# Optimization experiments

Measured on AMD Instinct MI355X. Metric: run time of the kernel, lower is better.

Reference implementation:

```python
import jax, jax.numpy as jnp
import numpy as np

N, C = 16384, 1000


def setup_inputs() -> dict:
    key = jax.random.key(0)
    ks = jax.random.split(key, 10)
    inp = {}
    for i in range(8):
        inp[f"outputs{i+1}"] = jax.random.normal(ks[i], (N, C), dtype=jnp.float32)
    inp["mimic"] = jax.random.normal(ks[8], (N, C), dtype=jnp.float32)
    inp["targets"] = jax.random.randint(ks[9], (N,), 0, C, dtype=jnp.int64)
    inp["n_test"] = N
    return inp


def _margin(x, targets):
    # top-2 margin, zeroed when target is not the argmax value
    top2, _ = jax.lax.top_k(x, 2)                      # [N, 2]
    tgt = jnp.take_along_axis(x, targets[:, None], axis=1)[:, 0]  # [N]
    return jnp.where(tgt == top2[:, 0], top2[:, 0] - top2[:, 1],
                     jnp.zeros((), x.dtype))


def reference(outputs1, outputs2, outputs3, outputs4, outputs5, outputs6,
              outputs7, outputs8, mimic, targets, n_test):
    T = 2.0
    outs = [outputs1, outputs2, outputs3, outputs4,
            outputs5, outputs6, outputs7, outputs8, mimic]
    margins = jnp.stack([_margin(o, targets) for o in outs], axis=1)  # [N, 9]
    out_threshold = jax.nn.softmax(margins / T, axis=1)               # [N, 9]
    max_preds = jnp.max(jnp.stack(outs[:8], axis=0))                  # scalar
    return (max_preds, out_threshold)
```

## Files before the change

### kernel.cpp

```cpp
#include <hip/hip_runtime.h>
#include <math.h>

#define BLOCK 256
#define WPB   (BLOCK / 64)

__global__ __launch_bounds__(BLOCK) void margin_kernel(
    const float* __restrict__ o0, const float* __restrict__ o1,
    const float* __restrict__ o2, const float* __restrict__ o3,
    const float* __restrict__ o4, const float* __restrict__ o5,
    const float* __restrict__ o6, const float* __restrict__ o7,
    const float* __restrict__ o8,
    const int* __restrict__ targets,
    float* __restrict__ out, float* __restrict__ block_max,
    int N, int C)
{
    __shared__ float s_m1[WPB][12];
    __shared__ float s_m2[WPB][12];

    const int tid  = threadIdx.x;
    const int lane = tid & 63;
    const int wib  = tid >> 6;
    const int row  = blockIdx.x;
    const int nf4  = C >> 2;
    const unsigned rowoff = (unsigned)row * (unsigned)C;

    float tvv = 0.0f;
    if (wib == 0 && lane < 9) {
        const int c = targets[row];
        const float* tp = o0;
        tp = (lane == 1) ? o1 : tp;  tp = (lane == 2) ? o2 : tp;
        tp = (lane == 3) ? o3 : tp;  tp = (lane == 4) ? o4 : tp;
        tp = (lane == 5) ? o5 : tp;  tp = (lane == 6) ? o6 : tp;
        tp = (lane == 7) ? o7 : tp;  tp = (lane == 8) ? o8 : tp;
        tvv = tp[rowoff + c];
    }

    float m1[9], m2[9];
    #pragma unroll
    for (int k = 0; k < 9; ++k) { m1[k] = -INFINITY; m2[k] = -INFINITY; }

    const float4* p[9] = {
        (const float4*)(o0 + rowoff), (const float4*)(o1 + rowoff),
        (const float4*)(o2 + rowoff), (const float4*)(o3 + rowoff),
        (const float4*)(o4 + rowoff), (const float4*)(o5 + rowoff),
        (const float4*)(o6 + rowoff), (const float4*)(o7 + rowoff),
        (const float4*)(o8 + rowoff) };

    for (int f4 = tid; f4 < nf4; f4 += BLOCK) {
        float4 v[9];
        #pragma unroll
        for (int k = 0; k < 9; ++k) v[k] = p[k][f4];
        #pragma unroll
        for (int k = 0; k < 9; ++k) {
            m2[k] = fmaxf(m2[k], fminf(m1[k], v[k].x)); m1[k] = fmaxf(m1[k], v[k].x);
            m2[k] = fmaxf(m2[k], fminf(m1[k], v[k].y)); m1[k] = fmaxf(m1[k], v[k].y);
            m2[k] = fmaxf(m2[k], fminf(m1[k], v[k].z)); m1[k] = fmaxf(m1[k], v[k].z);
            m2[k] = fmaxf(m2[k], fminf(m1[k], v[k].w)); m1[k] = fmaxf(m1[k], v[k].w);
        }
    }
    if (C & 3) {
        const float* b[9] = {o0,o1,o2,o3,o4,o5,o6,o7,o8};
        for (int idx = (nf4 << 2) + tid; idx < C; idx += BLOCK) {
            #pragma unroll
            for (int k = 0; k < 9; ++k) {
                float v = b[k][rowoff + idx];
                m2[k] = fmaxf(m2[k], fminf(m1[k], v)); m1[k] = fmaxf(m1[k], v);
            }
        }
    }

    #pragma unroll
    for (int off = 32; off > 0; off >>= 1) {
        #pragma unroll
        for (int k = 0; k < 9; ++k) {
            float a1 = __shfl_xor(m1[k], off);
            float a2 = __shfl_xor(m2[k], off);
            m2[k] = fmaxf(fmaxf(m2[k], a2), fminf(m1[k], a1));
            m1[k] = fmaxf(m1[k], a1);
        }
    }

    if (lane == 0) {
        #pragma unroll
        for (int k = 0; k < 9; ++k) { s_m1[wib][k] = m1[k]; s_m2[wib][k] = m2[k]; }
    }
    __syncthreads();

    if (wib == 0) {
        float a1 = -INFINITY, a2 = -INFINITY;
        if (lane < 9) {
            a1 = s_m1[0][lane]; a2 = s_m2[0][lane];
            #pragma unroll
            for (int w = 1; w < WPB; ++w) {
                float b1 = s_m1[w][lane], b2 = s_m2[w][lane];
                a2 = fmaxf(fmaxf(a2, b2), fminf(a1, b1));
                a1 = fmaxf(a1, b1);
            }
        }
        float mg = (lane < 9) ? ((tvv == a1) ? (a1 - a2) : 0.0f) : -INFINITY;

        float mm = mg;
        #pragma unroll
        for (int off = 8; off > 0; off >>= 1) mm = fmaxf(mm, __shfl_xor(mm, off));
        float ex = (lane < 9) ? expf((mg - mm) * 0.5f) : 0.0f;
        float sum = ex;
        #pragma unroll
        for (int off = 8; off > 0; off >>= 1) sum += __shfl_xor(sum, off);
        if (lane < 9)
            out[1 + (size_t)row * 9 + lane] = ex / sum;

        float g = (lane < 8) ? a1 : -INFINITY;
        #pragma unroll
        for (int off = 8; off > 0; off >>= 1) g = fmaxf(g, __shfl_xor(g, off));
        if (lane == 0) block_max[row] = g;
    }
}

__global__ __launch_bounds__(256) void finalize_kernel(
    const float* __restrict__ block_max, float* __restrict__ out, int n)
{
    __shared__ float s[4];
    const int lane = threadIdx.x & 63;
    float v = -INFINITY;
    for (int i = threadIdx.x; i < n; i += 256) v = fmaxf(v, block_max[i]);
    #pragma unroll
    for (int off = 32; off > 0; off >>= 1) v = fmaxf(v, __shfl_xor(v, off));
    if (lane == 0) s[threadIdx.x >> 6] = v;
    __syncthreads();
    if (threadIdx.x == 0)
        out[0] = fmaxf(fmaxf(s[0], s[1]), fmaxf(s[2], s[3]));
}

extern "C" void kernel_launch(void* const* d_in, const int* in_sizes, int n_in,
                              void* d_out, int out_size, void* d_ws, size_t ws_size,
                              hipStream_t stream) {
    const float* o0 = (const float*)d_in[0];
    const float* o1 = (const float*)d_in[1];
    const float* o2 = (const float*)d_in[2];
    const float* o3 = (const float*)d_in[3];
    const float* o4 = (const float*)d_in[4];
    const float* o5 = (const float*)d_in[5];
    const float* o6 = (const float*)d_in[6];
    const float* o7 = (const float*)d_in[7];
    const float* o8 = (const float*)d_in[8];
    const int* targets = (const int*)d_in[9];
    const int N = in_sizes[9];
    const int C = in_sizes[0] / N;
    float* out = (float*)d_out;
    float* block_max = (float*)d_ws;

    margin_kernel<<<dim3(N), dim3(BLOCK), 0, stream>>>(
        o0, o1, o2, o3, o4, o5, o6, o7, o8, targets, out, block_max, N, C);
    finalize_kernel<<<1, 256, 0, stream>>>(block_max, out, N);
}
```

Before: 498.8 us.

## Assign one wavefront per (row, array) pair and split softmax into separate pass

Work is remapped so each wavefront computes the top-2 margin of a single row of a single input array, instead of one block reducing all nine arrays for a row. Raw margins are written to the output, and a second kernel applies the per-row softmax while one extra block reduces the global max. The global max is gathered through atomicMax on order-preserving encoded floats spread over 4096 slots. The aim is to raise memory parallelism and cut register pressure from the nine parallel accumulators. In exchange it adds a memset, a second read and write of the output, and atomic traffic.

```diff
diff --git a/kernel.cpp b/kernel.cpp
--- a/kernel.cpp
+++ b/kernel.cpp
@@ -3,6 +3,18 @@
 
 #define BLOCK 256
 #define WPB   (BLOCK / 64)
+#define NSLOT 4096
+
+__device__ __forceinline__ unsigned enc_f32(float x) {
+    unsigned b = __float_as_uint(x);
+    return (b & 0x80000000u) ? ~b : (b | 0x80000000u);
+}
+__device__ __forceinline__ float dec_f32(unsigned u) {
+    unsigned b = (u & 0x80000000u) ? (u & 0x7fffffffu) : ~u;
+    return __uint_as_float(b);
+}
+
+#define TOP2_UPD(x) { m2 = fmaxf(m2, fminf(m1, (x))); m1 = fmaxf(m1, (x)); }
 
 __global__ __launch_bounds__(BLOCK) void margin_kernel(
     const float* __restrict__ o0, const float* __restrict__ o1,
@@ -11,124 +23,113 @@
     const float* __restrict__ o6, const float* __restrict__ o7,
     const float* __restrict__ o8,
     const int* __restrict__ targets,
-    float* __restrict__ out, float* __restrict__ block_max,
+    float* __restrict__ out, unsigned* __restrict__ slots,
     int N, int C)
 {
-    __shared__ float s_m1[WPB][12];
-    __shared__ float s_m2[WPB][12];
+    __shared__ float s_gm[WPB];
 
     const int tid  = threadIdx.x;
     const int lane = tid & 63;
     const int wib  = tid >> 6;
-    const int row  = blockIdx.x;
-    const int nf4  = C >> 2;
-    const unsigned rowoff = (unsigned)row * (unsigned)C;
 
-    float tvv = 0.0f;
-    if (wib == 0 && lane < 9) {
-        const int c = targets[row];
-        const float* tp = o0;
-        tp = (lane == 1) ? o1 : tp;  tp = (lane == 2) ? o2 : tp;
-        tp = (lane == 3) ? o3 : tp;  tp = (lane == 4) ? o4 : tp;
-        tp = (lane == 5) ? o5 : tp;  tp = (lane == 6) ? o6 : tp;
-        tp = (lane == 7) ? o7 : tp;  tp = (lane == 8) ? o8 : tp;
-        tvv = tp[rowoff + c];
-    }
+    const int pair  = __builtin_amdgcn_readfirstlane((int)blockIdx.x * WPB + wib);
+    const int valid = pair < N * 9;
+    const int row   = pair / 9;
+    const int arr   = pair - row * 9;
 
-    float m1[9], m2[9];
-    #pragma unroll
-    for (int k = 0; k < 9; ++k) { m1[k] = -INFINITY; m2[k] = -INFINITY; }
+    float m1 = -INFINITY, m2 = -INFINITY;
 
-    const float4* p[9] = {
-        (const float4*)(o0 + rowoff), (const float4*)(o1 + rowoff),
-        (const float4*)(o2 + rowoff), (const float4*)(o3 + rowoff),
-        (const float4*)(o4 + rowoff), (const float4*)(o5 + rowoff),
-        (const float4*)(o6 + rowoff), (const float4*)(o7 + rowoff),
-        (const float4*)(o8 + rowoff) };
+    if (valid) {
+        const float* bp = o0;
+        bp = (arr == 1) ? o1 : bp;  bp = (arr == 2) ? o2 : bp;
+        bp = (arr == 3) ? o3 : bp;  bp = (arr == 4) ? o4 : bp;
+        bp = (arr == 5) ? o5 : bp;  bp = (arr == 6) ? o6 : bp;
+        bp = (arr == 7) ? o7 : bp;  bp = (arr == 8) ? o8 : bp;
 
-    for (int f4 = tid; f4 < nf4; f4 += BLOCK) {
-        float4 v[9];
+        const unsigned rowoff = (unsigned)row * (unsigned)C;
+        const int c   = targets[row];
+        const float tvv = bp[rowoff + c];
+        const float4* p = (const float4*)(bp + rowoff);
+        const int nf4 = C >> 2;
+
+        int base = 0;
+        for (; base + 256 <= nf4; base += 256) {
+            float4 v0 = p[base + lane];
+            float4 v1 = p[base + lane + 64];
+            float4 v2 = p[base + lane + 128];
+            float4 v3 = p[base + lane + 192];
+            TOP2_UPD(v0.x) TOP2_UPD(v0.y) TOP2_UPD(v0.z) TOP2_UPD(v0.w)
+            TOP2_UPD(v1.x) TOP2_UPD(v1.y) TOP2_UPD(v1.z) TOP2_UPD(v1.w)
+            TOP2_UPD(v2.x) TOP2_UPD(v2.y) TOP2_UPD(v2.z) TOP2_UPD(v2.w)
+            TOP2_UPD(v3.x) TOP2_UPD(v3.y) TOP2_UPD(v3.z) TOP2_UPD(v3.w)
+        }
         #pragma unroll
-        for (int k = 0; k < 9; ++k) v[k] = p[k][f4];
+        for (int b = 0; b < 4; ++b) {
+            const int idx = base + b * 64 + lane;
+            float4 v = make_float4(-INFINITY, -INFINITY, -INFINITY, -INFINITY);
+            if (idx < nf4) v = p[idx];
+            TOP2_UPD(v.x) TOP2_UPD(v.y) TOP2_UPD(v.z) TOP2_UPD(v.w)
+        }
+        if (C & 3) {
+            const int idx = (nf4 << 2) + lane;
+            if (idx < C) { float v = (bp + rowoff)[idx]; TOP2_UPD(v) }
+        }
+
         #pragma unroll
-        for (int k = 0; k < 9; ++k) {
-            m2[k] = fmaxf(m2[k], fminf(m1[k], v[k].x)); m1[k] = fmaxf(m1[k], v[k].x);
-            m2[k] = fmaxf(m2[k], fminf(m1[k], v[k].y)); m1[k] = fmaxf(m1[k], v[k].y);
-            m2[k] = fmaxf(m2[k], fminf(m1[k], v[k].z)); m1[k] = fmaxf(m1[k], v[k].z);
-            m2[k] = fmaxf(m2[k], fminf(m1[k], v[k].w)); m1[k] = fmaxf(m1[k], v[k].w);
+        for (int off = 32; off > 0; off >>= 1) {
+            float a1 = __shfl_xor(m1, off);
+            float a2 = __shfl_xor(m2, off);
+            m2 = fmaxf(fmaxf(m2, a2), fminf(m1, a1));
+            m1 = fmaxf(m1, a1);
         }
-    }
-    if (C & 3) {
-        const float* b[9] = {o0,o1,o2,o3,o4,o5,o6,o7,o8};
-        for (int idx = (nf4 << 2) + tid; idx < C; idx += BLOCK) {
-            #pragma unroll
-            for (int k = 0; k < 9; ++k) {
-                float v = b[k][rowoff + idx];
-                m2[k] = fmaxf(m2[k], fminf(m1[k], v)); m1[k] = fmaxf(m1[k], v);
-            }
+
+        if (lane == 0) {
+            float mg = (tvv == m1) ? (m1 - m2) : 0.0f;
+            out[1 + (size_t)row * 9 + arr] = mg;
         }
     }
 
-    #pragma unroll
-    for (int off = 32; off > 0; off >>= 1) {
-        #pragma unroll
-        for (int k = 0; k < 9; ++k) {
-            float a1 = __shfl_xor(m1[k], off);
-            float a2 = __shfl_xor(m2[k], off);
-            m2[k] = fmaxf(fmaxf(m2[k], a2), fminf(m1[k], a1));
-            m1[k] = fmaxf(m1[k], a1);
-        }
-    }
-
-    if (lane == 0) {
-        #pragma unroll
-        for (int k = 0; k < 9; ++k) { s_m1[wib][k] = m1[k]; s_m2[wib][k] = m2[k]; }
-    }
+    if (lane == 0) s_gm[wib] = (valid && arr < 8) ? m1 : -INFINITY;
     __syncthreads();
-
-    if (wib == 0) {
-        float a1 = -INFINITY, a2 = -INFINITY;
-        if (lane < 9) {
-            a1 = s_m1[0][lane]; a2 = s_m2[0][lane];
-            #pragma unroll
-            for (int w = 1; w < WPB; ++w) {
-                float b1 = s_m1[w][lane], b2 = s_m2[w][lane];
-                a2 = fmaxf(fmaxf(a2, b2), fminf(a1, b1));
-                a1 = fmaxf(a1, b1);
-            }
-        }
-        float mg = (lane < 9) ? ((tvv == a1) ? (a1 - a2) : 0.0f) : -INFINITY;
-
-        float mm = mg;
-        #pragma unroll
-        for (int off = 8; off > 0; off >>= 1) mm = fmaxf(mm, __shfl_xor(mm, off));
-        float ex = (lane < 9) ? expf((mg - mm) * 0.5f) : 0.0f;
-        float sum = ex;
-        #pragma unroll
-        for (int off = 8; off > 0; off >>= 1) sum += __shfl_xor(sum, off);
-        if (lane < 9)
-            out[1 + (size_t)row * 9 + lane] = ex / sum;
-
-        float g = (lane < 8) ? a1 : -INFINITY;
-        #pragma unroll
-        for (int off = 8; off > 0; off >>= 1) g = fmaxf(g, __shfl_xor(g, off));
-        if (lane == 0) block_max[row] = g;
+    if (tid == 0) {
+        float g = fmaxf(fmaxf(s_gm[0], s_gm[1]), fmaxf(s_gm[2], s_gm[3]));
+        atomicMax(&slots[blockIdx.x & (NSLOT - 1)], enc_f32(g));
     }
 }
 
-__global__ __launch_bounds__(256) void finalize_kernel(
-    const float* __restrict__ block_max, float* __restrict__ out, int n)
+__global__ __launch_bounds__(256) void softmax_max_kernel(
+    float* __restrict__ out, const unsigned* __restrict__ slots, int N)
 {
-    __shared__ float s[4];
-    const int lane = threadIdx.x & 63;
-    float v = -INFINITY;
-    for (int i = threadIdx.x; i < n; i += 256) v = fmaxf(v, block_max[i]);
-    #pragma unroll
-    for (int off = 32; off > 0; off >>= 1) v = fmaxf(v, __shfl_xor(v, off));
-    if (lane == 0) s[threadIdx.x >> 6] = v;
-    __syncthreads();
-    if (threadIdx.x == 0)
-        out[0] = fmaxf(fmaxf(s[0], s[1]), fmaxf(s[2], s[3]));
+    if ((int)blockIdx.x == (int)gridDim.x - 1) {
+        __shared__ float s[4];
+        const int lane = threadIdx.x & 63;
+        float v = -INFINITY;
+        for (int i = threadIdx.x; i < NSLOT; i += 256)
+            v = fmaxf(v, dec_f32(slots[i]));
+        #pragma unroll
+        for (int off = 32; off > 0; off >>= 1) v = fmaxf(v, __shfl_xor(v, off));
+        if (lane == 0) s[threadIdx.x >> 6] = v;
+        __syncthreads();
+        if (threadIdx.x == 0)
+            out[0] = fmaxf(fmaxf(s[0], s[1]), fmaxf(s[2], s[3]));
+    } else {
+        const int row = (int)blockIdx.x * 256 + threadIdx.x;
+        if (row < N) {
+            const size_t base = 1 + (size_t)row * 9;
+            float m[9];
+            #pragma unroll
+            for (int k = 0; k < 9; ++k) m[k] = out[base + k];
+            float mm = m[0];
+            #pragma unroll
+            for (int k = 1; k < 9; ++k) mm = fmaxf(mm, m[k]);
+            float e[9], sum = 0.0f;
+            #pragma unroll
+            for (int k = 0; k < 9; ++k) { e[k] = expf((m[k] - mm) * 0.5f); sum += e[k]; }
+            const float inv = 1.0f / sum;
+            #pragma unroll
+            for (int k = 0; k < 9; ++k) out[base + k] = e[k] * inv;
+        }
+    }
 }
 
 extern "C" void kernel_launch(void* const* d_in, const int* in_sizes, int n_in,
@@ -147,9 +148,15 @@
     const int N = in_sizes[9];
     const int C = in_sizes[0] / N;
     float* out = (float*)d_out;
-    float* block_max = (float*)d_ws;
+    unsigned* slots = (unsigned*)d_ws;
 
-    margin_kernel<<<dim3(N), dim3(BLOCK), 0, stream>>>(
-        o0, o1, o2, o3, o4, o5, o6, o7, o8, targets, out, block_max, N, C);
-    finalize_kernel<<<1, 256, 0, stream>>>(block_max, out, N);
+    hipMemsetAsync(slots, 0, NSLOT * sizeof(unsigned), stream);
+
+    const int pairs = N * 9;
+    const int grid1 = (pairs + WPB - 1) / WPB;
+    margin_kernel<<<dim3(grid1), dim3(BLOCK), 0, stream>>>(
+        o0, o1, o2, o3, o4, o5, o6, o7, o8, targets, out, slots, N, C);
+
+    const int nsm = (N + 255) / 256;
+    softmax_max_kernel<<<dim3(nsm + 1), dim3(256), 0, stream>>>(out, slots, N);
 }
```

Result: no change. 494.4 us (-0.9%).
